# Kernel tuning notes

Hardware: AMD Instinct MI355X
Metric: run time of the kernel (lower is better)

Reference implementation:

```python
import jax, jax.numpy as jnp
import numpy as np

BETA = 0.25
STRIDE = 64  # LCCombine: ConvTranspose1d with ones kernel, kernel_size == stride


def setup_inputs() -> dict:
    key = jax.random.key(0)
    k0, k1, k2, k3 = jax.random.split(key, 4)
    B, Q, K, N = 2, 64, 512, 1024
    n_classes = 256
    n_wav = N * STRIDE - 1
    quant_pred = jax.random.normal(k0, (B, n_classes, n_wav), dtype=jnp.float32)
    ze = jax.random.normal(k1, (B, Q, N), dtype=jnp.float32)
    emb = jax.random.normal(k2, (K, N), dtype=jnp.float32)
    target_wav = jax.random.randint(k3, (B, 1, n_wav), 0, n_classes)
    return {"quant_pred": quant_pred, "ze": ze, "emb": emb, "target_wav": target_wav}


def _combine(x):
    # LCCombine: replicate each bottleneck-rate value over STRIDE wav steps
    # (transposed conv, ones kernel, kernel==stride), then drop last step.
    # x: (B, N) -> (B, 1, N*STRIDE - 1)
    return jnp.repeat(x, STRIDE, axis=-1)[:, None, :-1]


def reference(quant_pred, ze, emb, target_wav):
    # l2 loss: stop-grad on ze (codebook update term)
    sg_ze = jax.lax.stop_gradient(ze)
    d = sg_ze[:, :, None, :] - emb[None, None, :, :]      # (B, Q, K, N)
    l2_loss = jnp.min(jnp.sum(d * d, axis=1), axis=1)      # (B, N)
    # commitment loss: stop-grad on emb
    sg_emb = jax.lax.stop_gradient(emb)
    dc = ze[:, :, None, :] - sg_emb[None, None, :, :]      # (B, Q, K, N)
    com_loss = jnp.min(jnp.sum(dc * dc, axis=1), axis=1) * BETA  # (B, N)

    l2_loss_comb = _combine(l2_loss)                       # (B, 1, N_wav)
    com_loss_comb = _combine(com_loss)                     # (B, 1, N_wav)

    log_pred = jax.nn.log_softmax(quant_pred, axis=1)      # (B, C, N_wav)
    log_pred_target = jnp.take_along_axis(log_pred, target_wav, axis=1)  # (B,1,N_wav)

    total_loss_terms = log_pred_target + l2_loss_comb + com_loss_comb
    return jnp.mean(total_loss_terms)
```

## Files before the change

kernel.cpp:

```cpp
#include <hip/hip_runtime.h>


#define QQ   64
#define NN   1024
#define KK   512
#define CLS  256
#define NW   65535

__global__ __launch_bounds__(256) void vq_fused_kernel(
        const float* __restrict__ qp,
        const float* __restrict__ ze,
        const float* __restrict__ emb,
        const int*   __restrict__ tgt,
        float* __restrict__ out)
{
    const int g     = blockIdx.x * 256 + threadIdx.x;
    const int b     = g >> 16;
    const int t     = g & 0xFFFF;
    const bool valid = (t < NW);
    const int tc    = valid ? t : (NW - 1);
    const int n     = tc >> 6;
    const int lane  = threadIdx.x & 63;

    const float* p = qp + (size_t)b * CLS * NW + tc;

    int tg = tgt[(size_t)b * NW + tc];

    float cur[8];
    #pragma unroll
    for (int u = 0; u < 8; ++u) cur[u] = p[(size_t)u * NW];

    float v  = ze[(size_t)(b * QQ + lane) * NN + n];
    float s1 = v, s2 = v * v;
    #pragma unroll
    for (int msk = 32; msk >= 1; msk >>= 1) {
        s1 += __shfl_xor(s1, msk, 64);
        s2 += __shfl_xor(s2, msk, 64);
    }
    float best = 3.4e38f;
    float n2s1 = -2.0f * s1;
    #pragma unroll
    for (int j = 0; j < KK / 64; ++j) {
        float e = emb[(size_t)(lane + 64 * j) * NN + n];
        float cost = fmaf(e, fmaf((float)QQ, e, n2s1), s2);
        best = fminf(best, cost);
    }
    #pragma unroll
    for (int msk = 32; msk >= 1; msk >>= 1)
        best = fminf(best, __shfl_xor(best, msk, 64));
    const float l2 = 1.25f * best;

    float tv = p[(size_t)tg * NW];

    float m = -3.4e38f, s = 0.0f;
    auto merge8 = [&](const float* x) {
        float m01 = fmaxf(x[0], x[1]), m23 = fmaxf(x[2], x[3]);
        float m45 = fmaxf(x[4], x[5]), m67 = fmaxf(x[6], x[7]);
        float m8  = fmaxf(fmaxf(m01, m23), fmaxf(m45, m67));
        float s8  = __expf(x[0] - m8) + __expf(x[1] - m8)
                  + __expf(x[2] - m8) + __expf(x[3] - m8)
                  + __expf(x[4] - m8) + __expf(x[5] - m8)
                  + __expf(x[6] - m8) + __expf(x[7] - m8);
        float nm  = fmaxf(m, m8);
        s = s * __expf(m - nm) + s8 * __expf(m8 - nm);
        m = nm;
    };

    for (int c = 8; c < CLS; c += 8) {
        float nxt[8];
        #pragma unroll
        for (int u = 0; u < 8; ++u) nxt[u] = p[(size_t)(c + u) * NW];
        merge8(cur);
        #pragma unroll
        for (int u = 0; u < 8; ++u) cur[u] = nxt[u];
    }
    merge8(cur);

    float lse = m + __logf(s);
    float contrib = valid ? (tv - lse + l2) : 0.0f;

    #pragma unroll
    for (int msk = 32; msk >= 1; msk >>= 1)
        contrib += __shfl_xor(contrib, msk, 64);

    __shared__ float part[4];
    int wv = threadIdx.x >> 6;
    if (lane == 0) part[wv] = contrib;
    __syncthreads();
    if (threadIdx.x == 0) {
        float blk = part[0] + part[1] + part[2] + part[3];
        atomicAdd(out, blk * (1.0f / 131070.0f));
    }
}

extern "C" void kernel_launch(void* const* d_in, const int* in_sizes, int n_in,
                              void* d_out, int out_size, void* d_ws, size_t ws_size,
                              hipStream_t stream) {
    const float* quant_pred = (const float*)d_in[0];
    const float* ze         = (const float*)d_in[1];
    const float* emb        = (const float*)d_in[2];
    const int*   target     = (const int*)  d_in[3];
    float* out = (float*)d_out;
    (void)d_ws; (void)ws_size; (void)in_sizes; (void)n_in; (void)out_size;

    hipMemsetAsync(out, 0, sizeof(float), stream);
    vq_fused_kernel<<<512, 256, 0, stream>>>(quant_pred, ze, emb, target, out);
}
```

Baseline: 203.5 us.

## Split class reduction across two waves per position with double-buffered loads

Each block now handles 128 time positions with two waves per position group, each covering half of the 256 classes. The partial max/sum pairs are merged through shared memory. The grid doubles, and loads are double-buffered across two 8-wide register sets to raise memory-level parallelism on this bandwidth-bound log-softmax. The cost is an extra barrier and shared-memory exchange, and the VQ distance work is now done by only half the waves.

```diff
diff --git a/kernel.cpp b/kernel.cpp
--- a/kernel.cpp
+++ b/kernel.cpp
@@ -14,43 +14,50 @@
         const int*   __restrict__ tgt,
         float* __restrict__ out)
 {
-    const int g     = blockIdx.x * 256 + threadIdx.x;
-    const int b     = g >> 16;
-    const int t     = g & 0xFFFF;
+    const int lane = threadIdx.x & 63;
+    const int wv   = threadIdx.x >> 6;
+    const int half = wv >> 1;
+    const int posw = wv & 1;
+    const int g    = blockIdx.x * 128 + posw * 64 + lane;
+    const int b    = g >> 16;
+    const int t    = g & 0xFFFF;
     const bool valid = (t < NW);
-    const int tc    = valid ? t : (NW - 1);
-    const int n     = tc >> 6;
-    const int lane  = threadIdx.x & 63;
+    const int tc   = valid ? t : (NW - 1);
+    const int n    = tc >> 6;
 
     const float* p = qp + (size_t)b * CLS * NW + tc;
+    const int cb = half * 128;
 
-    int tg = tgt[(size_t)b * NW + tc];
+    float bufA[8], bufB[8];
+    #pragma unroll
+    for (int u = 0; u < 8; ++u) bufA[u] = p[(size_t)(cb + u) * NW];
+    #pragma unroll
+    for (int u = 0; u < 8; ++u) bufB[u] = p[(size_t)(cb + 8 + u) * NW];
 
-    float cur[8];
-    #pragma unroll
-    for (int u = 0; u < 8; ++u) cur[u] = p[(size_t)u * NW];
+    float tv = 0.0f, l2 = 0.0f;
+    if (half == 0) {
+        int tg = tgt[(size_t)b * NW + tc];
+        tv = p[(size_t)tg * NW];
 
-    float v  = ze[(size_t)(b * QQ + lane) * NN + n];
-    float s1 = v, s2 = v * v;
-    #pragma unroll
-    for (int msk = 32; msk >= 1; msk >>= 1) {
-        s1 += __shfl_xor(s1, msk, 64);
-        s2 += __shfl_xor(s2, msk, 64);
+        float v  = ze[(size_t)(b * QQ + lane) * NN + n];
+        float s1 = v, s2 = v * v;
+        #pragma unroll
+        for (int msk = 32; msk >= 1; msk >>= 1) {
+            s1 += __shfl_xor(s1, msk, 64);
+            s2 += __shfl_xor(s2, msk, 64);
+        }
+        float best = 3.4e38f;
+        float n2s1 = -2.0f * s1;
+        #pragma unroll
+        for (int j = 0; j < KK / 64; ++j) {
+            float e = emb[(size_t)(lane + 64 * j) * NN + n];
+            best = fminf(best, fmaf(e, fmaf((float)QQ, e, n2s1), s2));
+        }
+        #pragma unroll
+        for (int msk = 32; msk >= 1; msk >>= 1)
+            best = fminf(best, __shfl_xor(best, msk, 64));
+        l2 = 1.25f * best;
     }
-    float best = 3.4e38f;
-    float n2s1 = -2.0f * s1;
-    #pragma unroll
-    for (int j = 0; j < KK / 64; ++j) {
-        float e = emb[(size_t)(lane + 64 * j) * NN + n];
-        float cost = fmaf(e, fmaf((float)QQ, e, n2s1), s2);
-        best = fminf(best, cost);
-    }
-    #pragma unroll
-    for (int msk = 32; msk >= 1; msk >>= 1)
-        best = fminf(best, __shfl_xor(best, msk, 64));
-    const float l2 = 1.25f * best;
-
-    float tv = p[(size_t)tg * NW];
 
     float m = -3.4e38f, s = 0.0f;
     auto merge8 = [&](const float* x) {
@@ -66,31 +73,38 @@
         m = nm;
     };
 
-    for (int c = 8; c < CLS; c += 8) {
-        float nxt[8];
+    #pragma unroll
+    for (int k = 0; k < 14; k += 2) {
+        merge8(bufA);
         #pragma unroll
-        for (int u = 0; u < 8; ++u) nxt[u] = p[(size_t)(c + u) * NW];
-        merge8(cur);
+        for (int u = 0; u < 8; ++u) bufA[u] = p[(size_t)(cb + (k + 2) * 8 + u) * NW];
+        merge8(bufB);
         #pragma unroll
-        for (int u = 0; u < 8; ++u) cur[u] = nxt[u];
+        for (int u = 0; u < 8; ++u) bufB[u] = p[(size_t)(cb + (k + 3) * 8 + u) * NW];
     }
-    merge8(cur);
+    merge8(bufA);
+    merge8(bufB);
 
-    float lse = m + __logf(s);
-    float contrib = valid ? (tv - lse + l2) : 0.0f;
+    __shared__ float msh[128][2];
+    __shared__ float part[2];
+    const int pos = posw * 64 + lane;
+    if (half == 1) { msh[pos][0] = m; msh[pos][1] = s; }
+    __syncthreads();
 
-    #pragma unroll
-    for (int msk = 32; msk >= 1; msk >>= 1)
-        contrib += __shfl_xor(contrib, msk, 64);
-
-    __shared__ float part[4];
-    int wv = threadIdx.x >> 6;
-    if (lane == 0) part[wv] = contrib;
+    if (half == 0) {
+        float m1  = msh[pos][0], s1v = msh[pos][1];
+        float nm  = fmaxf(m, m1);
+        float ss  = s * __expf(m - nm) + s1v * __expf(m1 - nm);
+        float lse = nm + __logf(ss);
+        float contrib = valid ? (tv - lse + l2) : 0.0f;
+        #pragma unroll
+        for (int msk = 32; msk >= 1; msk >>= 1)
+            contrib += __shfl_xor(contrib, msk, 64);
+        if (lane == 0) part[wv] = contrib;
+    }
     __syncthreads();
-    if (threadIdx.x == 0) {
-        float blk = part[0] + part[1] + part[2] + part[3];
-        atomicAdd(out, blk * (1.0f / 131070.0f));
-    }
+    if (threadIdx.x == 0)
+        atomicAdd(out, (part[0] + part[1]) * (1.0f / 131070.0f));
 }
 
 extern "C" void kernel_launch(void* const* d_in, const int* in_sizes, int n_in,
@@ -104,5 +118,5 @@
     (void)d_ws; (void)ws_size; (void)in_sizes; (void)n_in; (void)out_size;
 
     hipMemsetAsync(out, 0, sizeof(float), stream);
-    vq_fused_kernel<<<512, 256, 0, stream>>>(quant_pred, ze, emb, target, out);
+    vq_fused_kernel<<<1024, 256, 0, stream>>>(quant_pred, ze, emb, target, out);
 }
```

Measured after the change: 204.1 us. Within noise of the previous version (+0.3%).
